# Kernel optimization log

Hardware: AMD Instinct MI355X
Metric: run time of the kernel (lower is better)

Reference implementation:

```python
import jax, jax.numpy as jnp
import numpy as np

WIDTH = 384
STEP_SIZE = 0.1  # hard-coded in EnergyBlock.__init__
EPS = 1e-5


def conv1d(x, w):
    # x: [B, Cin, L], w: [Cout, Cin, K], stride 1, SAME padding (padding=1 for k=3)
    return jax.lax.conv_general_dilated(
        x, w, window_strides=(1,), padding='SAME',
        dimension_numbers=('NCH', 'OIH', 'NCH'))


def layer_norm_cl(x):
    # torch layer_norm over shape[1:] == normalize jointly over (C, L) per batch elem,
    # no affine params, biased variance.
    mu = jnp.mean(x, axis=(1, 2), keepdims=True)
    var = jnp.mean(jnp.square(x - mu), axis=(1, 2), keepdims=True)
    return (x - mu) * jax.lax.rsqrt(var + EPS)


def energy_block(cat, op_w):
    # cat: [B, width+1, L] = concat(interim_thought, x)
    xl = layer_norm_cl(cat[:, :WIDTH])          # post-LN x (the grad variable)
    c = conv1d(cat, op_w)                        # operator(inputs): no path through xl
    # Ex = sum(c * xl) + sum(where(xl>=0, xl^2, 0))
    # dEx/dxl = c + 2*relu(xl)  (analytic; matches torch.autograd.grad)
    grads = c + 2.0 * jnp.maximum(xl, 0.0)
    return xl - STEP_SIZE * grads


def _init_conv(key, cout, cin, k=3):
    scale = (1.0 / (cin * k)) ** 0.5
    return jax.random.uniform(key, (cout, cin, k), jnp.float32, -scale, scale)


def setup_inputs() -> dict:
    key = jax.random.key(0)
    ks = jax.random.split(key, 6)
    B, L = 32, 512
    return {
        'x': jax.random.normal(ks[0], (B, 1, L), jnp.float32),
        'iters_to_do': 16,
        'proj_w': _init_conv(ks[1], WIDTH, 1),
        'op_w': _init_conv(ks[2], WIDTH, WIDTH + 1),
        'h1_w': _init_conv(ks[3], WIDTH, WIDTH),
        'h2_w': _init_conv(ks[4], WIDTH // 2, WIDTH),
        'h3_w': _init_conv(ks[5], 2, WIDTH // 2),
    }


def reference(x, iters_to_do, proj_w, op_w, h1_w, h2_w, h3_w):
    relu = jax.nn.relu
    interim = relu(conv1d(x, proj_w))  # initial_thought [B, width, L]

    def step(it, _):
        cat = jnp.concatenate([it, x], axis=1)       # recall=True
        new_it = energy_block(cat, op_w)
        out = conv1d(relu(conv1d(relu(conv1d(new_it, h1_w)), h2_w)), h3_w)  # [B,2,L]
        return new_it, out

    _, outs = jax.lax.scan(step, interim, None, length=iters_to_do)
    # eval mode: return all_outputs [B, iters, 2, L]
    return jnp.transpose(outs, (1, 0, 2, 3))
```

## Files before the change

### kernel.cpp

```cpp
#include <hip/hip_runtime.h>
#include <hip/hip_bf16.h>

#define BB 32
#define WW 384
#define LL 512
#define ITERS 16
#define NPB (WW * LL)
#define LROWS 514
#define RP (LROWS * 8)

typedef __attribute__((ext_vector_type(8))) short bf16x8;
typedef __attribute__((ext_vector_type(4))) float f32x4;

__device__ __forceinline__ float b2f(short s) {
    unsigned u = ((unsigned)(unsigned short)s) << 16;
    float f;
    __builtin_memcpy(&f, &u, 4);
    return f;
}
__device__ __forceinline__ short f2b(float v) {
    __hip_bfloat16 h = __float2bfloat16(v);
    return *(short*)&h;
}

__device__ __forceinline__ void gld16(const short* g, short* l) {
    __builtin_amdgcn_global_load_lds(
        (const __attribute__((address_space(1))) unsigned int*)g,
        (__attribute__((address_space(3))) unsigned int*)l, 16, 0, 0);
}

__global__ void wsplit_op(const float* __restrict__ w, short* __restrict__ wh) {
    int i = blockIdx.x * 256 + threadIdx.x;
    if (i >= 3 * 48 * 384 * 8) return;
    int e = i & 7, co = (i >> 3) % 384, oct = (i >> 3) / 384 % 48,
        tap = i / (8 * 384 * 48);
    int ci = oct * 8 + e;
    wh[i] = f2b(w[(co * 385 + ci) * 3 + tap]);
}

__global__ void wx_prep(const float* __restrict__ w, float* __restrict__ wx) {
    int i = blockIdx.x * 256 + threadIdx.x;
    if (i >= 3 * 384) return;
    int co = i % 384, tap = i / 384;
    wx[tap * 384 + co] = w[(co * 385 + 384) * 3 + tap];
}

__global__ void wsplit_h(const float* __restrict__ w, short* __restrict__ wh,
                         int COD, int CO_real) {
    int i = blockIdx.x * 256 + threadIdx.x;
    if (i >= 3 * 48 * COD * 8) return;
    int e = i & 7, co = (i >> 3) % COD, oct = (i >> 3) / COD % 48,
        tap = i / (8 * COD * 48);
    int ci = oct * 8 + e;
    float v = (co < CO_real) ? w[(co * 384 + ci) * 3 + tap] : 0.f;
    wh[i] = f2b(v);
}

__global__ void init_rows(short* itAh, short* itAl, short* itBh, short* itBl,
                          short* a1A, short* a1B, short* a2A, short* a2B) {
    int row = (blockIdx.x & 1) ? (LROWS - 1) : 0;
    int b = blockIdx.x >> 1;
    int tid = threadIdx.x;
    for (int i = tid; i < 48 * 8; i += 64) {
        size_t o = (size_t)b * 48 * RP + (size_t)(i >> 3) * RP + row * 8 + (i & 7);
        itAh[o] = 0; itAl[o] = 0; itBh[o] = 0; itBl[o] = 0;
        a1A[o] = 0; a1B[o] = 0;
    }
    for (int i = tid; i < 24 * 8; i += 64) {
        size_t o = (size_t)b * 24 * RP + (size_t)(i >> 3) * RP + row * 8 + (i & 7);
        a2A[o] = 0; a2B[o] = 0;
    }
}

__global__ void zero_part(float* part, int n) {
    int i = blockIdx.x * 256 + threadIdx.x;
    if (i < n) part[i] = 0.f;
}

__global__ __launch_bounds__(256) void proj_relu(const float* __restrict__ x,
                                                 const float* __restrict__ wp,
                                                 short* __restrict__ oh,
                                                 short* __restrict__ ol,
                                                 float* __restrict__ part) {
    int low3 = blockIdx.x & 7, r0 = blockIdx.x >> 3;
    int sl_lo = r0 & 3, chi = r0 >> 2;
    int c3 = chi * 8 + low3;
    int b = c3 >> 1, sl = ((c3 & 1) << 2) | sl_lo;
    int tid = threadIdx.x;
    __shared__ float ws[WW * 3];
    __shared__ float xs[66];
    for (int i = tid; i < WW * 3; i += 256) ws[i] = wp[i];
    int l0 = sl * 64;
    for (int i = tid; i < 66; i += 256) {
        int l = l0 + i - 1;
        xs[i] = (l >= 0 && l < LL) ? x[b * LL + l] : 0.f;
    }
    __syncthreads();
    size_t sb = (size_t)b * 48 * RP;
    float s = 0.f, sq = 0.f;
    for (int idx = tid; idx < 64 * WW; idx += 256) {
        int lo = idx / WW, co = idx % WW;
        float v = fmaxf(ws[co * 3] * xs[lo] + ws[co * 3 + 1] * xs[lo + 1] +
                            ws[co * 3 + 2] * xs[lo + 2], 0.f);
        size_t o = sb + (size_t)(co >> 3) * RP + (l0 + lo + 1) * 8 + (co & 7);
        __hip_bfloat16 h = __float2bfloat16(v);
        oh[o] = *(short*)&h;
        ol[o] = f2b(v - __bfloat162float(h));
        s += v; sq += v * v;
    }
    #pragma unroll
    for (int off = 32; off > 0; off >>= 1) {
        s += __shfl_down(s, off);
        sq += __shfl_down(sq, off);
    }
    __shared__ float sr[8];
    int w = tid >> 6;
    if ((tid & 63) == 0) { sr[w] = s; sr[4 + w] = sq; }
    __syncthreads();
    if (tid == 0) {
        atomicAdd(&part[b * 2], sr[0] + sr[1] + sr[2] + sr[3]);
        atomicAdd(&part[b * 2 + 1], sr[4] + sr[5] + sr[6] + sr[7]);
    }
}


#define MMAC(A, B, MT, NT)                                                 \
    acc[MT][NT] = __builtin_amdgcn_mfma_f32_16x16x32_bf16(A, B,            \
                                                          acc[MT][NT], 0, 0, 0);

#define STAGE(KC, TB)                                                      \
    do {                                                                   \
        short* sb_ = smem + (TB) * ASZ;                                    \
        _Pragma("unroll")                                                  \
        for (int r_ = 0; r_ < (ANS + 3) / 4; r_++) {                       \
            int s_ = r_ * 4 + wn;                                          \
            if (s_ < ANS) {                                                \
                int u0_ = s_ * 64;                                         \
                if (u0_ > AU - 64) u0_ = AU - 64;                          \
                int u_ = u0_ + lane;                                       \
                int oc_ = u_ / TLROWS;                                     \
                int rw_ = u_ - oc_ * TLROWS;                               \
                gld16(inh + ibase + (size_t)((KC) * 4 + oc_) * RP +        \
                          (size_t)(l0 + rw_) * 8,                          \
                      sb_ + u0_ * 8);                                      \
            }                                                              \
        }                                                                  \
    } while (0)

#define DECL_B(S) bf16x8 fb0##S, fb1##S, fb2##S, fb3##S;

#define LOADB(S, T, KC)                                                    \
    do {                                                                   \
        const short* bp_ = wh + ((((size_t)(T) * CHUNKS + (KC)) * 4 + q) * \
                                     COD + co0w + lane15) * 8;             \
        fb0##S = *(const bf16x8*)(bp_);                                    \
        fb1##S = *(const bf16x8*)(bp_ + 16 * 8);                           \
        fb2##S = *(const bf16x8*)(bp_ + 32 * 8);                           \
        fb3##S = *(const bf16x8*)(bp_ + 48 * 8);                           \
    } while (0)

#define COMP_TAP(SB, T, S)                                                 \
    do {                                                                   \
        const short* As_ = (SB);                                           \
        int ar_ = q * TLROWS + wl + lane15 + (T);                          \
        bf16x8 fa0 = *(const bf16x8*)(As_ + ar_ * 8);                      \
        bf16x8 fa1 = *(const bf16x8*)(As_ + (ar_ + 16) * 8);               \
        bf16x8 fa2 = *(const bf16x8*)(As_ + (ar_ + 32) * 8);               \
        bf16x8 fa3 = *(const bf16x8*)(As_ + (ar_ + 48) * 8);               \
        MMAC(fa0, fb0##S, 0, 0) MMAC(fa0, fb1##S, 0, 1)                    \
        MMAC(fa0, fb2##S, 0, 2) MMAC(fa0, fb3##S, 0, 3)                    \
        MMAC(fa1, fb0##S, 1, 0) MMAC(fa1, fb1##S, 1, 1)                    \
        MMAC(fa1, fb2##S, 1, 2) MMAC(fa1, fb3##S, 1, 3)                    \
        MMAC(fa2, fb0##S, 2, 0) MMAC(fa2, fb1##S, 2, 1)                    \
        MMAC(fa2, fb2##S, 2, 2) MMAC(fa2, fb3##S, 2, 3)                    \
        MMAC(fa3, fb0##S, 3, 0) MMAC(fa3, fb1##S, 3, 1)                    \
        MMAC(fa3, fb2##S, 3, 2) MMAC(fa3, fb3##S, 3, 3)                    \
    } while (0)

template <int CHUNKS, int IOCT, int OOCT, int COD, int MODE, int LSPLIT>
__device__ __forceinline__ void conv_body(
    int bid, short* smem,
    const short* __restrict__ inh, const short* __restrict__ inl,
    const short* __restrict__ wh, const float* __restrict__ xf,
    const float* __restrict__ wx, const float* __restrict__ part_in,
    float* __restrict__ part_out, short* __restrict__ outh,
    short* __restrict__ outl) {
    constexpr int TLROWS = LSPLIT ? 258 : 130;
    constexpr int ASZ = 4 * TLROWS * 8;
    constexpr int AU = 4 * TLROWS;
    constexpr int ANS = (AU + 63) / 64;

    int tid = threadIdx.x;
    int lane = tid & 63;
    int wn = __builtin_amdgcn_readfirstlane(tid >> 6);
    int lane15 = lane & 15, q = lane >> 4;
    int b, l0, co0, wl, wco;
    if (LSPLIT) {
        int low3 = bid & 7, r0 = bid >> 3;
        int ct = r0 % 3, chi = r0 / 3;
        int c2 = chi * 8 + low3;
        b = c2 >> 1; l0 = (c2 & 1) * 256; co0 = ct * 64;
        wl = wn * 64; wco = 0;
    } else {
        int low3 = bid & 7, r0 = bid >> 3;
        int ct = r0 % 3, s2 = r0 / 3;
        int ltlo = s2 & 1, chi = s2 >> 1;
        int c = chi * 8 + low3;
        b = c >> 1;
        int lt = ((c & 1) << 1) | ltlo;
        l0 = lt * 128; co0 = ct * 128;
        wl = (wn >> 1) * 64; wco = (wn & 1) * 64;
    }
    const int co0w = co0 + wco;
    const size_t ibase = (size_t)b * IOCT * RP;

    f32x4 acc[4][4];
    #pragma unroll
    for (int i = 0; i < 4; i++)
        #pragma unroll
        for (int j = 0; j < 4; j++) acc[i][j] = (f32x4){0.f, 0.f, 0.f, 0.f};

    DECL_B(X)
    DECL_B(Y)
    DECL_B(Z)
    STAGE(0, 0);
    LOADB(X, 0, 0);
    LOADB(Y, 1, 0);
    __syncthreads();
    #pragma unroll 2
    for (int kc = 0; kc < CHUNKS; kc++) {
        int cur = kc & 1;
        LOADB(Z, 2, kc);
        if (kc + 1 < CHUNKS) STAGE(kc + 1, cur ^ 1);
        short* sb = smem + cur * ASZ;
        COMP_TAP(sb, 0, X);
        if (kc + 1 < CHUNKS) LOADB(X, 0, kc + 1);
        COMP_TAP(sb, 1, Y);
        if (kc + 1 < CHUNKS) LOADB(Y, 1, kc + 1);
        COMP_TAP(sb, 2, Z);
        __syncthreads();
    }

    int l0w = l0 + wl;
    const size_t obase = (size_t)b * OOCT * RP;
    if constexpr (MODE == 1) {
        float s_in = part_in[b * 2], sq_in = part_in[b * 2 + 1];
        float mu = s_in / (float)NPB;
        float var = sq_in / (float)NPB - mu * mu;
        float rs = rsqrtf(var + 1e-5f);
        const float* xb = xf + b * LL;
        float s = 0.f, sq = 0.f;
        #pragma unroll
        for (int nt = 0; nt < 4; nt++) {
            int n = co0w + nt * 16 + lane15;
            float w0 = wx[n], w1 = wx[384 + n], w2 = wx[768 + n];
            #pragma unroll
            for (int mt = 0; mt < 4; mt++)
                #pragma unroll
                for (int r = 0; r < 4; r++) {
                    int m = mt * 16 + q * 4 + r;
                    int l = l0w + m;
                    size_t idx = ibase + (size_t)(n >> 3) * RP +
                                 (l + 1) * 8 + (n & 7);
                    float xm1 = (l > 0) ? xb[l - 1] : 0.f;
                    float xp1 = (l < LL - 1) ? xb[l + 1] : 0.f;
                    float c = acc[mt][nt][r] + w0 * xm1 + w1 * xb[l] + w2 * xp1;
                    float itv = b2f(inh[idx]) + b2f(inl[idx]);
                    float xl = (itv - mu) * rs;
                    float nv = xl - 0.1f * c - 0.2f * fmaxf(xl, 0.f);
                    s += nv;
                    sq += nv * nv;
                    __hip_bfloat16 h = __float2bfloat16(nv);
                    outh[idx] = *(short*)&h;
                    outl[idx] = f2b(nv - __bfloat162float(h));
                }
        }
        #pragma unroll
        for (int off = 32; off > 0; off >>= 1) {
            s += __shfl_down(s, off);
            sq += __shfl_down(sq, off);
        }
        __shared__ float sr[8];
        if (lane == 0) { sr[wn] = s; sr[4 + wn] = sq; }
        __syncthreads();
        if (tid == 0) {
            atomicAdd(&part_out[b * 2], sr[0] + sr[1] + sr[2] + sr[3]);
            atomicAdd(&part_out[b * 2 + 1], sr[4] + sr[5] + sr[6] + sr[7]);
        }
    } else {
        #pragma unroll
        for (int mt = 0; mt < 4; mt++)
            #pragma unroll
            for (int nt = 0; nt < 4; nt++)
                #pragma unroll
                for (int r = 0; r < 4; r++) {
                    int m = mt * 16 + q * 4 + r;
                    int n = co0w + nt * 16 + lane15;
                    size_t idx = obase + (size_t)(n >> 3) * RP +
                                 (l0w + m + 1) * 8 + (n & 7);
                    outh[idx] = f2b(fmaxf(acc[mt][nt][r], 0.f));
                }
    }
}

__global__ __launch_bounds__(128) void h3k(const short* __restrict__ a2,
                                           const float* __restrict__ w3,
                                           float* __restrict__ out, int t) {
    __shared__ float ws3[2 * 192 * 3];
    int tid = threadIdx.x;
    for (int i = tid; i < 2 * 192 * 3; i += 128) ws3[i] = w3[i];
    __syncthreads();
    int low3 = blockIdx.x & 7, r0 = blockIdx.x >> 3;
    int sl_lo = r0 & 3, chi = r0 >> 2;
    int c3 = chi * 8 + low3;
    int b = c3 >> 1, sl = ((c3 & 1) << 2) | sl_lo;
    int l = sl * 64 + (tid >> 1);
    int ch = tid & 1;
    const short* ab = a2 + (size_t)b * 24 * RP;
    const float* wc = ws3 + ch * 576;
    float a = 0.f;
    #pragma unroll 4
    for (int oct = 0; oct < 24; oct++) {
        const short* p = ab + (size_t)oct * RP + l * 8;
        bf16x8 v0 = *(const bf16x8*)p;
        bf16x8 v1 = *(const bf16x8*)(p + 8);
        bf16x8 v2 = *(const bf16x8*)(p + 16);
        #pragma unroll
        for (int j = 0; j < 8; j++) {
            const float* wp = wc + (oct * 8 + j) * 3;
            a += wp[0] * b2f(v0[j]) + wp[1] * b2f(v1[j]) + wp[2] * b2f(v2[j]);
        }
    }
    out[(((size_t)b * ITERS + t) * 2 + ch) * LL + l] = a;
}

__global__ __launch_bounds__(256, 3) void fusedF(
    const short* __restrict__ ch, const short* __restrict__ cl,
    short* __restrict__ nh, short* __restrict__ nl,
    const short* __restrict__ wOph, const short* __restrict__ wH1,
    const short* __restrict__ wH2, const float* __restrict__ xf,
    const float* __restrict__ wx, const float* __restrict__ part_in,
    float* __restrict__ part_out, short* __restrict__ a1w,
    const short* __restrict__ a1r, short* __restrict__ a2w,
    int opB, int h1B) {
    __shared__ __align__(16) short smem[2 * 4 * 258 * 8];
    int bid = blockIdx.x;
    if (bid < opB) {
        conv_body<12, 48, 48, 384, 1, 0>(bid, smem, ch, cl, wOph, xf, wx,
                                         part_in, part_out, nh, nl);
    } else if (bid < opB + h1B) {
        conv_body<12, 48, 48, 384, 0, 0>(bid - opB, smem, ch, nullptr, wH1,
                                         nullptr, nullptr, nullptr, nullptr,
                                         a1w, nullptr);
    } else {
        conv_body<12, 48, 24, 192, 0, 1>(bid - opB - h1B, smem, a1r, nullptr,
                                         wH2, nullptr, nullptr, nullptr,
                                         nullptr, a2w, nullptr);
    }
}

extern "C" void kernel_launch(void* const* d_in, const int* in_sizes, int n_in,
                              void* d_out, int out_size, void* d_ws, size_t ws_size,
                              hipStream_t stream) {
    const float* x = (const float*)d_in[0];
    const float* proj_w = (const float*)d_in[2];
    const float* op_w = (const float*)d_in[3];
    const float* h1_w = (const float*)d_in[4];
    const float* h2_w = (const float*)d_in[5];
    const float* h3_w = (const float*)d_in[6];
    float* out = (float*)d_out;

    char* base = (char*)d_ws;
    size_t off = 0;
    auto alloc = [&](size_t bytes) {
        char* p = base + off;
        off += (bytes + 255) & ~(size_t)255;
        return p;
    };
    const size_t ITB = (size_t)BB * 48 * RP * 2;
    short* itAh = (short*)alloc(ITB);
    short* itAl = (short*)alloc(ITB);
    short* itBh = (short*)alloc(ITB);
    short* itBl = (short*)alloc(ITB);
    short* a1A = (short*)alloc((size_t)BB * 48 * RP * 2);
    short* a1B = (short*)alloc((size_t)BB * 48 * RP * 2);
    short* a2A = (short*)alloc((size_t)BB * 24 * RP * 2);
    short* a2B = (short*)alloc((size_t)BB * 24 * RP * 2);
    short* wOph = (short*)alloc((size_t)3 * 48 * 384 * 8 * 2);
    short* wH1 = (short*)alloc((size_t)3 * 48 * 384 * 8 * 2);
    short* wH2 = (short*)alloc((size_t)3 * 48 * 192 * 8 * 2);
    float* wx = (float*)alloc((size_t)3 * 384 * 4);
    float* part = (float*)alloc((size_t)(ITERS + 1) * 64 * 4);
    if (off > ws_size) return;

    wsplit_op<<<(3 * 48 * 384 * 8 + 255) / 256, 256, 0, stream>>>(op_w, wOph);
    wx_prep<<<5, 256, 0, stream>>>(op_w, wx);
    wsplit_h<<<(3 * 48 * 384 * 8 + 255) / 256, 256, 0, stream>>>(h1_w, wH1, 384, 384);
    wsplit_h<<<(3 * 48 * 192 * 8 + 255) / 256, 256, 0, stream>>>(h2_w, wH2, 192, 192);
    init_rows<<<BB * 2, 64, 0, stream>>>(itAh, itAl, itBh, itBl, a1A, a1B,
                                         a2A, a2B);
    zero_part<<<5, 256, 0, stream>>>(part, (ITERS + 1) * 64);
    proj_relu<<<BB * 8, 256, 0, stream>>>(x, proj_w, itAh, itAl, part);

    short* a1buf[2] = {a1A, a1B};
    short* a2buf[2] = {a2A, a2B};
    short *ch = itAh, *cl = itAl, *nh = itBh, *nl = itBl;
    for (int t = 0; t < ITERS + 2; t++) {
        int opB = (t < ITERS) ? 384 : 0;
        int h1B = (t >= 1 && t <= ITERS) ? 384 : 0;
        int h2B = (t >= 2 && t <= ITERS + 1) ? 192 : 0;
        int tp = (t < ITERS) ? t : 0;
        fusedF<<<opB + h1B + h2B, 256, 0, stream>>>(
            ch, cl, nh, nl, wOph, wH1, wH2, x, wx, part + tp * 64,
            part + (tp + 1) * 64, a1buf[(t - 1) & 1], a1buf[(t - 2) & 1],
            a2buf[(t - 2) & 1], opB, h1B);
        if (t >= 3)
            h3k<<<256, 128, 0, stream>>>(a2buf[(t - 3) & 1], h3_w, out, t - 3);
        if (t < ITERS) {
            short* th = ch; ch = nh; nh = th;
            short* tl = cl; cl = nl; nl = tl;
        }
    }
    h3k<<<256, 128, 0, stream>>>(a2buf[(ITERS - 1) & 1], h3_w, out, ITERS - 1);
}
```

Measured before the change: 1.058 ms.

## Relax loop barrier to partial vmcnt wait and fuse h3 conv into fused launch

Replaces __syncthreads in the conv main loop with an s_waitcnt vmcnt(8) plus s_barrier, letting some outstanding global loads stay in flight across the barrier. Also moves the final 2-channel h3 conv into the fused kernel as extra 256-thread blocks, adding one more pipeline stage and removing the separate per-iteration launches. The partial wait risks an LDS race if staged loads are not among the completed ones.

```diff
diff --git a/kernel.cpp b/kernel.cpp
--- a/kernel.cpp
+++ b/kernel.cpp
@@ -123,6 +123,14 @@
     }
 }
 
+
+#define PIPE_BARRIER()                                                     \
+    do {                                                                   \
+        asm volatile("s_waitcnt vmcnt(8)" ::: "memory");                   \
+        __builtin_amdgcn_sched_barrier(0);                                 \
+        __builtin_amdgcn_s_barrier();                                      \
+        __builtin_amdgcn_sched_barrier(0);                                 \
+    } while (0)
 
 #define MMAC(A, B, MT, NT)                                                 \
     acc[MT][NT] = __builtin_amdgcn_mfma_f32_16x16x32_bf16(A, B,            \
@@ -226,7 +234,7 @@
     STAGE(0, 0);
     LOADB(X, 0, 0);
     LOADB(Y, 1, 0);
-    __syncthreads();
+    PIPE_BARRIER();
     #pragma unroll 2
     for (int kc = 0; kc < CHUNKS; kc++) {
         int cur = kc & 1;
@@ -238,7 +246,7 @@
         COMP_TAP(sb, 1, Y);
         if (kc + 1 < CHUNKS) LOADB(Y, 1, kc + 1);
         COMP_TAP(sb, 2, Z);
-        __syncthreads();
+        PIPE_BARRIER();
     }
 
     int l0w = l0 + wl;
@@ -303,18 +311,20 @@
     }
 }
 
-__global__ __launch_bounds__(128) void h3k(const short* __restrict__ a2,
-                                           const float* __restrict__ w3,
-                                           float* __restrict__ out, int t) {
-    __shared__ float ws3[2 * 192 * 3];
+__device__ __forceinline__ void h3_body(int bid, short* smem,
+                                        const short* __restrict__ a2,
+                                        const float* __restrict__ w3,
+                                        float* __restrict__ out, int t) {
+    float* ws3 = (float*)smem;
     int tid = threadIdx.x;
-    for (int i = tid; i < 2 * 192 * 3; i += 128) ws3[i] = w3[i];
+    for (int i = tid; i < 2 * 192 * 3; i += 256) ws3[i] = w3[i];
     __syncthreads();
-    int low3 = blockIdx.x & 7, r0 = blockIdx.x >> 3;
-    int sl_lo = r0 & 3, chi = r0 >> 2;
-    int c3 = chi * 8 + low3;
-    int b = c3 >> 1, sl = ((c3 & 1) << 2) | sl_lo;
-    int l = sl * 64 + (tid >> 1);
+    int low3 = bid & 7, r0 = bid >> 3;
+    int qlo = r0 & 1, chi = r0 >> 1;
+    int c = chi * 8 + low3;
+    int b = c >> 1;
+    int qq = ((c & 1) << 1) | qlo;
+    int l = qq * 128 + (tid >> 1);
     int ch = tid & 1;
     const short* ab = a2 + (size_t)b * 24 * RP;
     const float* wc = ws3 + ch * 576;
@@ -342,7 +352,8 @@
     const float* __restrict__ wx, const float* __restrict__ part_in,
     float* __restrict__ part_out, short* __restrict__ a1w,
     const short* __restrict__ a1r, short* __restrict__ a2w,
-    int opB, int h1B) {
+    const short* __restrict__ a2r, const float* __restrict__ w3,
+    float* __restrict__ out, int th3, int opB, int h1B, int h2B) {
     __shared__ __align__(16) short smem[2 * 4 * 258 * 8];
     int bid = blockIdx.x;
     if (bid < opB) {
@@ -352,10 +363,12 @@
         conv_body<12, 48, 48, 384, 0, 0>(bid - opB, smem, ch, nullptr, wH1,
                                          nullptr, nullptr, nullptr, nullptr,
                                          a1w, nullptr);
-    } else {
+    } else if (bid < opB + h1B + h2B) {
         conv_body<12, 48, 24, 192, 0, 1>(bid - opB - h1B, smem, a1r, nullptr,
                                          wH2, nullptr, nullptr, nullptr,
                                          nullptr, a2w, nullptr);
+    } else {
+        h3_body(bid - opB - h1B - h2B, smem, a2r, w3, out, th3);
     }
 }
 
@@ -405,21 +418,20 @@
     short* a1buf[2] = {a1A, a1B};
     short* a2buf[2] = {a2A, a2B};
     short *ch = itAh, *cl = itAl, *nh = itBh, *nl = itBl;
-    for (int t = 0; t < ITERS + 2; t++) {
+    for (int t = 0; t < ITERS + 3; t++) {
         int opB = (t < ITERS) ? 384 : 0;
         int h1B = (t >= 1 && t <= ITERS) ? 384 : 0;
         int h2B = (t >= 2 && t <= ITERS + 1) ? 192 : 0;
+        int h3B = (t >= 3 && t <= ITERS + 2) ? 128 : 0;
         int tp = (t < ITERS) ? t : 0;
-        fusedF<<<opB + h1B + h2B, 256, 0, stream>>>(
+        fusedF<<<opB + h1B + h2B + h3B, 256, 0, stream>>>(
             ch, cl, nh, nl, wOph, wH1, wH2, x, wx, part + tp * 64,
             part + (tp + 1) * 64, a1buf[(t - 1) & 1], a1buf[(t - 2) & 1],
-            a2buf[(t - 2) & 1], opB, h1B);
-        if (t >= 3)
-            h3k<<<256, 128, 0, stream>>>(a2buf[(t - 3) & 1], h3_w, out, t - 3);
+            a2buf[(t - 2) & 1], a2buf[(t + 1) & 1], h3_w, out, t - 3,
+            opB, h1B, h2B);
         if (t < ITERS) {
             short* th = ch; ch = nh; nh = th;
             short* tl = cl; cl = nl; nl = tl;
         }
     }
-    h3k<<<256, 128, 0, stream>>>(a2buf[(ITERS - 1) & 1], h3_w, out, ITERS - 1);
-}
+}
```

New measurement: 953.6 us. 1.11x faster.
